# Kernel tuning notes

Measured on AMD Instinct MI355X. Metric: run time of the kernel, lower is better.

## Reference

```python
import jax, jax.numpy as jnp
import numpy as np

B, S, D = 4, 2048, 1024

def setup_inputs() -> dict:
    key = jax.random.key(0)
    k1, k2, k3, k4 = jax.random.split(key, 4)
    scale = 1.0 / np.sqrt(D)
    return {
        "X": jax.random.normal(k1, (B, S, D), dtype=jnp.float32),
        "W_Q": jax.random.normal(k2, (D, D), dtype=jnp.float32) * scale,
        "W_K": jax.random.normal(k3, (D, D), dtype=jnp.float32) * scale,
        "W_V": jax.random.normal(k4, (D, D), dtype=jnp.float32) * scale,
    }

def reference(X, W_Q, W_K, W_V):
    # nn.Linear computes X @ W.T; weights stored as [out, in]
    Q = jnp.einsum('bsd,ed->bse', X, W_Q)
    K = jnp.einsum('bsd,ed->bse', X, W_K)
    V = jnp.einsum('bsd,ed->bse', X, W_V)
    d_model = X.shape[-1]
    scores = jnp.einsum('bqd,bkd->bqk', Q, K) / jnp.sqrt(jnp.float32(d_model))
    S_len = X.shape[1]
    causal = jnp.tril(jnp.ones((S_len, S_len), dtype=bool))  # True = keep
    scores = jnp.where(causal[None, :, :], scores, -jnp.inf)
    attn = jax.nn.softmax(scores, axis=-1)
    return jnp.einsum('bqk,bkd->bqd', attn, V)
```

## Files before the change

kernel.cpp:

```cpp
#include <hip/hip_runtime.h>

typedef unsigned short u16;
typedef __attribute__((ext_vector_type(8))) short short8;
typedef __attribute__((ext_vector_type(4))) float floatx4;
typedef __attribute__((ext_vector_type(4))) unsigned short ushortx4;

#define BATCH 4
#define SEQ   2048
#define DMODEL 1024

__device__ __forceinline__ u16 f2bf(float f) {
  unsigned int u = __builtin_bit_cast(unsigned int, f);
  u = (u + 0x7FFFu + ((u >> 16) & 1u)) >> 16;
  return (u16)u;
}
__device__ __forceinline__ float bf2f(u16 u) {
  unsigned int v = ((unsigned int)u) << 16;
  return __builtin_bit_cast(float, v);
}

typedef const __attribute__((address_space(1))) unsigned int as1_u32;
typedef __attribute__((address_space(3))) unsigned int as3_u32;

__device__ __forceinline__ void gload16(const void* gp, void* lp) {
  __builtin_amdgcn_global_load_lds((as1_u32*)gp, (as3_u32*)lp, 16, 0, 0);
}

#define CFENCE asm volatile("" ::: "memory")
#define LGKM0  do { asm volatile("s_waitcnt lgkmcnt(0)" ::: "memory"); \
                    __builtin_amdgcn_sched_barrier(0); } while (0)
#define VMC(n) asm volatile("s_waitcnt vmcnt(" #n ")" ::: "memory")
#define BAR    __builtin_amdgcn_s_barrier()
#define PRIO1  __builtin_amdgcn_s_setprio(1)
#define PRIO0  __builtin_amdgcn_s_setprio(0)

template<int NW, int STRIPE>
__device__ __forceinline__ void stage_unit(
    const u16* __restrict__ G, int ld, int org, int kt, int h,
    u16* region, int w, int l)
{
  constexpr int CPS = STRIPE / 16;
  const int lr = l >> 3, s = l & 7;
  #pragma unroll
  for (int i = 0; i < 2; ++i) {
    int c = i * NW + w;
    int R = (c / CPS) * STRIPE + h * (STRIPE / 2) + (c % CPS) * 8;
    const u16* src = G + (size_t)(org + R + lr) * ld + kt * 64 + ((s ^ lr) << 3);
    gload16(src, region + R * 64);
  }
}

template<int REP>
__device__ __forceinline__ short8 rdfrag(const u16* region, int wq, int m, int kh, int l) {
  int r = wq * (REP * 16) + m * 16 + (l & 15);
  int c = kh * 32 + ((l >> 4) << 3);
  return *(const short8*)(region + ((r * 64 + c) ^ ((r & 7) << 3)));
}

template<int WM, int WN, int MREP, int NREP>
__device__ __forceinline__ void gemm_core3(
    const u16* __restrict__ A, int lda,
    const u16* __restrict__ B, int ldb,
    int m0, int n0, int NT, u16* lds,
    floatx4 (&acc)[MREP][NREP])
{
  constexpr int NW = WM * WN;
  constexpr int BM = WM * MREP * 16, BN = WN * NREP * 16;
  constexpr int ABUF = BM * 64;
  constexpr int BUFSZ = (BM + BN) * 64;
  constexpr int MH = MREP / 2, NH = NREP / 2;
  constexpr int SA = BM / WM, SB = BN / WN;

  const int tid = threadIdx.x;
  const int w = tid >> 6, l = tid & 63;
  const int wr = w / WN, wc = w % WN;

  u16* buf0 = lds;
  u16* buf1 = lds + BUFSZ;

  stage_unit<NW, SA>(A, lda, m0, 0, 0, buf0, w, l);
  stage_unit<NW, SB>(B, ldb, n0, 0, 0, buf0 + ABUF, w, l);
  stage_unit<NW, SB>(B, ldb, n0, 0, 1, buf0 + ABUF, w, l);
  stage_unit<NW, SA>(A, lda, m0, 0, 1, buf0, w, l);
  stage_unit<NW, SA>(A, lda, m0, 1, 0, buf1, w, l);
  stage_unit<NW, SB>(B, ldb, n0, 1, 0, buf1 + ABUF, w, l);
  VMC(8);
  BAR;
  CFENCE;

  for (int kt = 0; kt < NT; ++kt) {
    u16* cur = (kt & 1) ? buf1 : buf0;
    u16* oth = (kt & 1) ? buf0 : buf1;
    const int t1 = (kt + 1 < NT) ? kt + 1 : NT - 1;
    const int t2 = (kt + 2 < NT) ? kt + 2 : NT - 1;

    short8 aLo[MH][2], aHi[MH][2], bLo[NH][2], bHi[NH][2];

    #pragma unroll
    for (int m = 0; m < MH; ++m)
      #pragma unroll
      for (int k = 0; k < 2; ++k) aLo[m][k] = rdfrag<MREP>(cur, wr, m, k, l);
    #pragma unroll
    for (int n = 0; n < NH; ++n)
      #pragma unroll
      for (int k = 0; k < 2; ++k) bLo[n][k] = rdfrag<NREP>(cur + ABUF, wc, n, k, l);
    stage_unit<NW, SB>(B, ldb, n0, t1, 1, oth + ABUF, w, l);
    stage_unit<NW, SA>(A, lda, m0, t1, 1, oth, w, l);
    VMC(10);
    LGKM0;
    BAR;
    CFENCE;
    PRIO1;
    #pragma unroll
    for (int m = 0; m < MH; ++m)
      #pragma unroll
      for (int n = 0; n < NH; ++n)
        #pragma unroll
        for (int k = 0; k < 2; ++k)
          acc[m][n] = __builtin_amdgcn_mfma_f32_16x16x32_bf16(aLo[m][k], bLo[n][k], acc[m][n], 0, 0, 0);
    PRIO0;

    #pragma unroll
    for (int n = 0; n < NH; ++n)
      #pragma unroll
      for (int k = 0; k < 2; ++k) bHi[n][k] = rdfrag<NREP>(cur + ABUF, wc, n + NH, k, l);
    stage_unit<NW, SA>(A, lda, m0, t2, 0, cur, w, l);
    VMC(10);
    LGKM0;
    BAR;
    CFENCE;
    PRIO1;
    #pragma unroll
    for (int m = 0; m < MH; ++m)
      #pragma unroll
      for (int n = 0; n < NH; ++n)
        #pragma unroll
        for (int k = 0; k < 2; ++k)
          acc[m][n + NH] = __builtin_amdgcn_mfma_f32_16x16x32_bf16(aLo[m][k], bHi[n][k], acc[m][n + NH], 0, 0, 0);
    PRIO0;

    #pragma unroll
    for (int m = 0; m < MH; ++m)
      #pragma unroll
      for (int k = 0; k < 2; ++k) aHi[m][k] = rdfrag<MREP>(cur, wr, m + MH, k, l);
    stage_unit<NW, SB>(B, ldb, n0, t2, 0, cur + ABUF, w, l);
    VMC(8);
    LGKM0;
    BAR;
    CFENCE;
    PRIO1;
    #pragma unroll
    for (int m = 0; m < MH; ++m)
      #pragma unroll
      for (int n = 0; n < NH; ++n)
        #pragma unroll
        for (int k = 0; k < 2; ++k) {
          acc[m + MH][n + NH] = __builtin_amdgcn_mfma_f32_16x16x32_bf16(aHi[m][k], bHi[n][k], acc[m + MH][n + NH], 0, 0, 0);
          acc[m + MH][n] = __builtin_amdgcn_mfma_f32_16x16x32_bf16(aHi[m][k], bLo[n][k], acc[m + MH][n], 0, 0, 0);
        }
    PRIO0;
  }
  VMC(0);
}

template<int WM, int WN, int MREP, int NREP>
__device__ __forceinline__ void gemm_core8(
    const u16* __restrict__ A, int lda,
    const u16* __restrict__ B, int ldb,
    int m0, int n0, int NT, u16* lds,
    floatx4 (&acc)[MREP][NREP])
{
  constexpr int NW = WM * WN;
  constexpr int BM = WM * MREP * 16, BN = WN * NREP * 16;
  constexpr int ABUF = BM * 64;
  constexpr int BUFSZ = (BM + BN) * 64;
  constexpr int MH = MREP / 2, NH = NREP / 2;
  constexpr int SA = BM / WM, SB = BN / WN;

  const int tid = threadIdx.x;
  const int w = tid >> 6, l = tid & 63;
  const int wr = w / WN, wc = w % WN;

  u16* const bufp[2] = { lds, lds + BUFSZ };

  stage_unit<NW, SA>(A, lda, m0, 0, 0, bufp[0], w, l);
  stage_unit<NW, SB>(B, ldb, n0, 0, 0, bufp[0] + ABUF, w, l);
  stage_unit<NW, SB>(B, ldb, n0, 0, 1, bufp[0] + ABUF, w, l);
  stage_unit<NW, SA>(A, lda, m0, 0, 1, bufp[0], w, l);
  stage_unit<NW, SA>(A, lda, m0, 1, 0, bufp[1], w, l);
  stage_unit<NW, SB>(B, ldb, n0, 1, 0, bufp[1] + ABUF, w, l);
  stage_unit<NW, SB>(B, ldb, n0, 1, 1, bufp[1] + ABUF, w, l);
  VMC(6);
  BAR;
  CFENCE;

  for (int t = 0; t < NT; t += 2) {
    u16* c0 = bufp[t & 1];
    u16* c1 = bufp[(t + 1) & 1];
    const int t2 = (t + 2 < NT) ? t + 2 : NT - 1;
    const int t3 = (t + 3 < NT) ? t + 3 : NT - 1;

    short8 aLo[MH][2], aHi[MH][2], bLo[NH][2], bHi[NH][2];

    #pragma unroll
    for (int m = 0; m < MH; ++m)
      #pragma unroll
      for (int k = 0; k < 2; ++k) aLo[m][k] = rdfrag<MREP>(c0, wr, m, k, l);
    #pragma unroll
    for (int n = 0; n < NH; ++n)
      #pragma unroll
      for (int k = 0; k < 2; ++k) bLo[n][k] = rdfrag<NREP>(c0 + ABUF, wc, n, k, l);
    stage_unit<NW, SA>(A, lda, m0, t + 1, 1, c1, w, l);
    if constexpr (MH * 2 + NH * 2 >= 12) asm volatile("s_waitcnt lgkmcnt(8)" ::: "memory");
    BAR; LGKM0; PRIO1;
    #pragma unroll
    for (int m = 0; m < MH; ++m)
      #pragma unroll
      for (int n = 0; n < NH; ++n)
        #pragma unroll
        for (int k = 0; k < 2; ++k)
          acc[m][n] = __builtin_amdgcn_mfma_f32_16x16x32_bf16(aLo[m][k], bLo[n][k], acc[m][n], 0, 0, 0);
    PRIO0; BAR; CFENCE;

    #pragma unroll
    for (int n = 0; n < NH; ++n)
      #pragma unroll
      for (int k = 0; k < 2; ++k) bHi[n][k] = rdfrag<NREP>(c0 + ABUF, wc, n + NH, k, l);
    stage_unit<NW, SA>(A, lda, m0, t2, 0, c0, w, l);
    BAR; LGKM0; PRIO1;
    #pragma unroll
    for (int m = 0; m < MH; ++m)
      #pragma unroll
      for (int n = 0; n < NH; ++n)
        #pragma unroll
        for (int k = 0; k < 2; ++k)
          acc[m][n + NH] = __builtin_amdgcn_mfma_f32_16x16x32_bf16(aLo[m][k], bHi[n][k], acc[m][n + NH], 0, 0, 0);
    PRIO0; BAR; CFENCE;

    #pragma unroll
    for (int m = 0; m < MH; ++m)
      #pragma unroll
      for (int k = 0; k < 2; ++k) aHi[m][k] = rdfrag<MREP>(c0, wr, m + MH, k, l);
    stage_unit<NW, SB>(B, ldb, n0, t2, 0, c0 + ABUF, w, l);
    BAR; LGKM0; PRIO1;
    #pragma unroll
    for (int m = 0; m < MH; ++m)
      #pragma unroll
      for (int n = 0; n < NH; ++n)
        #pragma unroll
        for (int k = 0; k < 2; ++k)
          acc[m + MH][n + NH] = __builtin_amdgcn_mfma_f32_16x16x32_bf16(aHi[m][k], bHi[n][k], acc[m + MH][n + NH], 0, 0, 0);
    PRIO0; BAR; CFENCE;

    stage_unit<NW, SB>(B, ldb, n0, t2, 1, c0 + ABUF, w, l);
    VMC(6);
    BAR; PRIO1;
    #pragma unroll
    for (int m = 0; m < MH; ++m)
      #pragma unroll
      for (int n = 0; n < NH; ++n)
        #pragma unroll
        for (int k = 0; k < 2; ++k)
          acc[m + MH][n] = __builtin_amdgcn_mfma_f32_16x16x32_bf16(aHi[m][k], bLo[n][k], acc[m + MH][n], 0, 0, 0);
    PRIO0; BAR; CFENCE;

    #pragma unroll
    for (int m = 0; m < MH; ++m)
      #pragma unroll
      for (int k = 0; k < 2; ++k) aLo[m][k] = rdfrag<MREP>(c1, wr, m, k, l);
    #pragma unroll
    for (int n = 0; n < NH; ++n)
      #pragma unroll
      for (int k = 0; k < 2; ++k) bLo[n][k] = rdfrag<NREP>(c1 + ABUF, wc, n, k, l);
    stage_unit<NW, SA>(A, lda, m0, t2, 1, c0, w, l);
    if constexpr (MH * 2 + NH * 2 >= 12) asm volatile("s_waitcnt lgkmcnt(8)" ::: "memory");
    BAR; LGKM0; PRIO1;
    #pragma unroll
    for (int m = 0; m < MH; ++m)
      #pragma unroll
      for (int n = 0; n < NH; ++n)
        #pragma unroll
        for (int k = 0; k < 2; ++k)
          acc[m][n] = __builtin_amdgcn_mfma_f32_16x16x32_bf16(aLo[m][k], bLo[n][k], acc[m][n], 0, 0, 0);
    PRIO0; BAR; CFENCE;

    #pragma unroll
    for (int n = 0; n < NH; ++n)
      #pragma unroll
      for (int k = 0; k < 2; ++k) bHi[n][k] = rdfrag<NREP>(c1 + ABUF, wc, n + NH, k, l);
    stage_unit<NW, SA>(A, lda, m0, t3, 0, c1, w, l);
    BAR; LGKM0; PRIO1;
    #pragma unroll
    for (int m = 0; m < MH; ++m)
      #pragma unroll
      for (int n = 0; n < NH; ++n)
        #pragma unroll
        for (int k = 0; k < 2; ++k)
          acc[m][n + NH] = __builtin_amdgcn_mfma_f32_16x16x32_bf16(aLo[m][k], bHi[n][k], acc[m][n + NH], 0, 0, 0);
    PRIO0; BAR; CFENCE;

    #pragma unroll
    for (int m = 0; m < MH; ++m)
      #pragma unroll
      for (int k = 0; k < 2; ++k) aHi[m][k] = rdfrag<MREP>(c1, wr, m + MH, k, l);
    stage_unit<NW, SB>(B, ldb, n0, t3, 0, c1 + ABUF, w, l);
    BAR; LGKM0; PRIO1;
    #pragma unroll
    for (int m = 0; m < MH; ++m)
      #pragma unroll
      for (int n = 0; n < NH; ++n)
        #pragma unroll
        for (int k = 0; k < 2; ++k)
          acc[m + MH][n + NH] = __builtin_amdgcn_mfma_f32_16x16x32_bf16(aHi[m][k], bHi[n][k], acc[m + MH][n + NH], 0, 0, 0);
    PRIO0; BAR; CFENCE;

    stage_unit<NW, SB>(B, ldb, n0, t3, 1, c1 + ABUF, w, l);
    VMC(6);
    BAR; PRIO1;
    #pragma unroll
    for (int m = 0; m < MH; ++m)
      #pragma unroll
      for (int n = 0; n < NH; ++n)
        #pragma unroll
        for (int k = 0; k < 2; ++k)
          acc[m + MH][n] = __builtin_amdgcn_mfma_f32_16x16x32_bf16(aHi[m][k], bLo[n][k], acc[m + MH][n], 0, 0, 0);
    PRIO0; BAR; CFENCE;
  }
  VMC(0);
}

__global__ __launch_bounds__(256)
void convert_k(const float* __restrict__ X,
               const float* __restrict__ WQ,
               const float* __restrict__ WK,
               const float* __restrict__ WV,
               u16* __restrict__ Xb, u16* __restrict__ Wb)
{
  const int NX = (BATCH*SEQ*DMODEL) / 4;
  const int NW_ = (DMODEL*DMODEL) / 4;
  const int total = NX + 3*NW_;
  for (int i = blockIdx.x * 256 + threadIdx.x; i < total; i += gridDim.x * 256) {
    const float4* src; u16* dst; int j;
    if (i < NX) { src = (const float4*)X; j = i; dst = Xb; }
    else {
      int t = i - NX; int w = t / NW_; j = t - w * NW_;
      src = (const float4*)(w == 0 ? WQ : (w == 1 ? WK : WV));
      dst = Wb + (size_t)w * (DMODEL*DMODEL);
    }
    float4 v = src[j];
    ushortx4 p = { f2bf(v.x), f2bf(v.y), f2bf(v.z), f2bf(v.w) };
    *(ushortx4*)(dst + (size_t)j * 4) = p;
  }
}

__global__ __launch_bounds__(512, 1)
void qk256(const u16* __restrict__ Xb, const u16* __restrict__ Wb,
           u16* __restrict__ Q, u16* __restrict__ K)
{
  __shared__ __align__(16) u16 lds[2 * (256 + 256) * 64];
  const int id = blockIdx.x;
  const int sw = (id & 7) * 32 + (id >> 3);
  const int z = sw >> 7;
  const int rem = sw & 127;
  const int mt = rem >> 2, nt = rem & 3;
  const int m0 = mt * 256, n0 = nt * 256;

  floatx4 acc[8][4] = {};
  gemm_core3<2, 4, 8, 4>(Xb, DMODEL, Wb + (size_t)z * DMODEL * DMODEL, DMODEL,
                         m0, n0, DMODEL / 64, lds, acc);

  const int l = threadIdx.x & 63, w = threadIdx.x >> 6;
  const int wr = w >> 2, wc = w & 3;
  const int row0 = m0 + wr * 128 + ((l >> 4) << 2);
  const int col0 = n0 + wc * 64 + (l & 15);
  u16* O = z ? K : Q;
  #pragma unroll
  for (int m = 0; m < 8; ++m)
    #pragma unroll
    for (int n = 0; n < 4; ++n)
      #pragma unroll
      for (int i = 0; i < 4; ++i)
        O[(size_t)(row0 + m*16 + i) * DMODEL + col0 + n*16] = f2bf(acc[m][n][i]);
}

__global__ __launch_bounds__(256, 2)
void sv128(const u16* __restrict__ Xb, const u16* __restrict__ Wb,
           const u16* __restrict__ Qb, const u16* __restrict__ Kb,
           u16* __restrict__ Sc, u16* __restrict__ Vt)
{
  __shared__ __align__(16) u16 lds[2 * (128 + 128) * 64];
  const int id = blockIdx.x;
  const int sw = (id & 7) * 132 + (id >> 3);

  const u16 *A, *B;
  int m0, n0, b = 0;
  bool is_s;
  if (sw < 544) {
    is_s = true;
    b = sw / 136;
    const int t = sw % 136;
    int qt = 0;
    while ((qt + 1) * (qt + 2) / 2 <= t) ++qt;
    const int kt = t - qt * (qt + 1) / 2;
    m0 = qt * 128; n0 = kt * 128;
    A = Qb + (size_t)b * SEQ * DMODEL;
    B = Kb + (size_t)b * SEQ * DMODEL;
  } else {
    is_s = false;
    const int s = sw - 544;
    m0 = (s >> 3) * 128; n0 = (s & 7) * 128;
    A = Xb;
    B = Wb + (size_t)2 * DMODEL * DMODEL;
  }

  floatx4 acc[4][4] = {};
  gemm_core8<2, 2, 4, 4>(A, DMODEL, B, DMODEL, m0, n0, DMODEL / 64, lds, acc);

  const int l = threadIdx.x & 63, w = threadIdx.x >> 6;
  const int wr = w >> 1, wc = w & 1;
  const int row0 = m0 + wr * 64 + ((l >> 4) << 2);
  const int col0 = n0 + wc * 64 + (l & 15);

  if (is_s) {
    u16* S = Sc + (size_t)b * SEQ * SEQ;
    #pragma unroll
    for (int m = 0; m < 4; ++m)
      #pragma unroll
      for (int n = 0; n < 4; ++n)
        #pragma unroll
        for (int i = 0; i < 4; ++i)
          S[(size_t)(row0 + m*16 + i) * SEQ + col0 + n*16] = f2bf(acc[m][n][i] * 0.03125f);
  } else {
    #pragma unroll
    for (int m = 0; m < 4; ++m) {
      int gm = row0 + m*16;
      int bb = gm >> 11, s2 = gm & (SEQ - 1);
      #pragma unroll
      for (int n = 0; n < 4; ++n) {
        int d = col0 + n*16;
        ushortx4 p = { f2bf(acc[m][n][0]), f2bf(acc[m][n][1]),
                       f2bf(acc[m][n][2]), f2bf(acc[m][n][3]) };
        *(ushortx4*)(Vt + ((size_t)bb * DMODEL + d) * SEQ + s2) = p;
      }
    }
  }
}

__global__ __launch_bounds__(256)
void softmax1p(u16* __restrict__ Sc)
{
  __shared__ float red[4];
  const int rg = blockIdx.x;
  const int q = rg & (SEQ - 1);
  u16* row = Sc + (size_t)rg * SEQ;
  const int t = threadIdx.x;
  const int lane = t & 63, wave = t >> 6;
  const int n = q + 1;
  const int kpad = ((q >> 7) + 1) << 7;
  const int k0 = t * 8;

  short8 v8 = {};
  if (k0 < kpad) v8 = *(const short8*)(row + k0);
  float f[8];
  float lmax = -3.4e38f;
  #pragma unroll
  for (int j = 0; j < 8; ++j) {
    f[j] = bf2f((u16)v8[j]);
    if (k0 + j < n) lmax = fmaxf(lmax, f[j]);
  }
  #pragma unroll
  for (int off = 32; off >= 1; off >>= 1)
    lmax = fmaxf(lmax, __shfl_xor(lmax, off));
  if (lane == 0) red[wave] = lmax;
  __syncthreads();
  const float rmax = fmaxf(fmaxf(red[0], red[1]), fmaxf(red[2], red[3]));
  __syncthreads();

  float lsum = 0.f;
  #pragma unroll
  for (int j = 0; j < 8; ++j) {
    float e = (k0 + j < n) ? __expf(f[j] - rmax) : 0.f;
    f[j] = e;
    lsum += e;
  }
  #pragma unroll
  for (int off = 32; off >= 1; off >>= 1)
    lsum += __shfl_xor(lsum, off);
  if (lane == 0) red[wave] = lsum;
  __syncthreads();
  const float inv = 1.f / (red[0] + red[1] + red[2] + red[3]);

  if (k0 < kpad) {
    short8 o;
    #pragma unroll
    for (int j = 0; j < 8; ++j) o[j] = (short)f2bf(f[j] * inv);
    *(short8*)(row + k0) = o;
  }
}

__global__ __launch_bounds__(256, 2)
void out128(const u16* __restrict__ Sc, const u16* __restrict__ Vt,
            float* __restrict__ Out)
{
  __shared__ __align__(16) u16 lds[2 * (128 + 128) * 64];
  const int id = blockIdx.x;
  const int j = id & 255;
  const int upper = id >> 8;
  const int qt = upper ? (15 - (j & 15)) : (j & 15);
  const int nt = (j >> 4) & 7;
  const int b  = (upper << 1) | (j >> 7);
  const int m0 = qt * 128, n0 = nt * 128;

  const u16* P = Sc + (size_t)b * SEQ * SEQ;
  const u16* V = Vt + (size_t)b * DMODEL * SEQ;
  const int NT = (qt + 1) * 2;

  floatx4 acc[4][4] = {};
  gemm_core8<2, 2, 4, 4>(P, SEQ, V, SEQ, m0, n0, NT, lds, acc);

  float* O = Out + (size_t)b * SEQ * DMODEL;
  const int l = threadIdx.x & 63, w = threadIdx.x >> 6;
  const int wr = w >> 1, wc = w & 1;
  const int row0 = m0 + wr * 64 + ((l >> 4) << 2);
  const int col0 = n0 + wc * 64 + (l & 15);
  #pragma unroll
  for (int m = 0; m < 4; ++m)
    #pragma unroll
    for (int n = 0; n < 4; ++n)
      #pragma unroll
      for (int i = 0; i < 4; ++i)
        O[(size_t)(row0 + m*16 + i) * DMODEL + col0 + n*16] = acc[m][n][i];
}

extern "C" void kernel_launch(void* const* d_in, const int* in_sizes, int n_in,
                              void* d_out, int out_size, void* d_ws, size_t ws_size,
                              hipStream_t stream)
{
  const float* X  = (const float*)d_in[0];
  const float* WQ = (const float*)d_in[1];
  const float* WK = (const float*)d_in[2];
  const float* WV = (const float*)d_in[3];
  float* Out = (float*)d_out;

  char* ws = (char*)d_ws;
  u16*   Xb = (u16*)(ws);
  u16*   Wb = (u16*)(ws + 16777216);
  u16*   Qb = (u16*)(ws + 23068672);
  u16*   Kb = (u16*)(ws + 39845888);
  u16*   Vt = (u16*)(ws + 56623104);
  u16*   Sc = (u16*)(ws + 73400320);

  convert_k<<<dim3(2048), dim3(256), 0, stream>>>(X, WQ, WK, WV, Xb, Wb);
  qk256<<<dim3(256), dim3(512), 0, stream>>>(Xb, Wb, Qb, Kb);
  sv128<<<dim3(1056), dim3(256), 0, stream>>>(Xb, Wb, Qb, Kb, Sc, Vt);
  softmax1p<<<dim3(BATCH * SEQ), dim3(256), 0, stream>>>(Sc);
  out128<<<dim3(512), dim3(256), 0, stream>>>(Sc, Vt, Out);
}
```

Before: 135.2 us.

## Replace 8-wave ping-pong GEMM core with simple K=32 double-buffered loop

Replaces the hand-scheduled ping-pong GEMM core (64-wide K tiles, staged quarter loads, interleaved barriers) in the S/V and output GEMM kernels with a simpler loop over 32-wide K tiles. Each iteration prefetches the next tile and runs 16 MFMAs per wave. LDS per block is halved and launch bounds are raised to 4 blocks per CU to gain occupancy. In exchange it gives up the fine-grained load/compute interleaving, and with half the work per barrier the synchronisation cost per FLOP goes up.

```diff
diff --git a/kernel.cpp b/kernel.cpp
--- a/kernel.cpp
+++ b/kernel.cpp
@@ -163,170 +163,71 @@
   VMC(0);
 }
 
-template<int WM, int WN, int MREP, int NREP>
-__device__ __forceinline__ void gemm_core8(
+__device__ __forceinline__ void stage32(
+    const u16* __restrict__ G, int ld, int org, int kt,
+    u16* region, int w, int l)
+{
+  const int lr = l >> 2, s = l & 3;
+  #pragma unroll
+  for (int i = 0; i < 2; ++i) {
+    int R = (i * 4 + w) * 16;
+    const u16* src = G + (size_t)(org + R + lr) * ld + kt * 32 + ((s ^ (lr & 3)) << 3);
+    gload16(src, region + R * 32);
+  }
+}
+
+__device__ __forceinline__ short8 rdfrag32(const u16* region, int wq, int m, int l) {
+  int r = wq * 64 + m * 16 + (l & 15);
+  int j = l >> 4;
+  return *(const short8*)(region + r * 32 + (((j ^ (r & 3))) << 3));
+}
+
+__device__ __forceinline__ void gemm_core32(
     const u16* __restrict__ A, int lda,
     const u16* __restrict__ B, int ldb,
     int m0, int n0, int NT, u16* lds,
-    floatx4 (&acc)[MREP][NREP])
-{
-  constexpr int NW = WM * WN;
-  constexpr int BM = WM * MREP * 16, BN = WN * NREP * 16;
-  constexpr int ABUF = BM * 64;
-  constexpr int BUFSZ = (BM + BN) * 64;
-  constexpr int MH = MREP / 2, NH = NREP / 2;
-  constexpr int SA = BM / WM, SB = BN / WN;
-
+    floatx4 (&acc)[4][4])
+{
+  constexpr int ABUF = 128 * 32;
+  constexpr int BUFSZ = 256 * 32;
   const int tid = threadIdx.x;
   const int w = tid >> 6, l = tid & 63;
-  const int wr = w / WN, wc = w % WN;
-
-  u16* const bufp[2] = { lds, lds + BUFSZ };
-
-  stage_unit<NW, SA>(A, lda, m0, 0, 0, bufp[0], w, l);
-  stage_unit<NW, SB>(B, ldb, n0, 0, 0, bufp[0] + ABUF, w, l);
-  stage_unit<NW, SB>(B, ldb, n0, 0, 1, bufp[0] + ABUF, w, l);
-  stage_unit<NW, SA>(A, lda, m0, 0, 1, bufp[0], w, l);
-  stage_unit<NW, SA>(A, lda, m0, 1, 0, bufp[1], w, l);
-  stage_unit<NW, SB>(B, ldb, n0, 1, 0, bufp[1] + ABUF, w, l);
-  stage_unit<NW, SB>(B, ldb, n0, 1, 1, bufp[1] + ABUF, w, l);
-  VMC(6);
-  BAR;
-  CFENCE;
-
-  for (int t = 0; t < NT; t += 2) {
-    u16* c0 = bufp[t & 1];
-    u16* c1 = bufp[(t + 1) & 1];
-    const int t2 = (t + 2 < NT) ? t + 2 : NT - 1;
-    const int t3 = (t + 3 < NT) ? t + 3 : NT - 1;
-
-    short8 aLo[MH][2], aHi[MH][2], bLo[NH][2], bHi[NH][2];
-
-    #pragma unroll
-    for (int m = 0; m < MH; ++m)
-      #pragma unroll
-      for (int k = 0; k < 2; ++k) aLo[m][k] = rdfrag<MREP>(c0, wr, m, k, l);
-    #pragma unroll
-    for (int n = 0; n < NH; ++n)
-      #pragma unroll
-      for (int k = 0; k < 2; ++k) bLo[n][k] = rdfrag<NREP>(c0 + ABUF, wc, n, k, l);
-    stage_unit<NW, SA>(A, lda, m0, t + 1, 1, c1, w, l);
-    if constexpr (MH * 2 + NH * 2 >= 12) asm volatile("s_waitcnt lgkmcnt(8)" ::: "memory");
-    BAR; LGKM0; PRIO1;
-    #pragma unroll
-    for (int m = 0; m < MH; ++m)
-      #pragma unroll
-      for (int n = 0; n < NH; ++n)
-        #pragma unroll
-        for (int k = 0; k < 2; ++k)
-          acc[m][n] = __builtin_amdgcn_mfma_f32_16x16x32_bf16(aLo[m][k], bLo[n][k], acc[m][n], 0, 0, 0);
-    PRIO0; BAR; CFENCE;
-
-    #pragma unroll
-    for (int n = 0; n < NH; ++n)
-      #pragma unroll
-      for (int k = 0; k < 2; ++k) bHi[n][k] = rdfrag<NREP>(c0 + ABUF, wc, n + NH, k, l);
-    stage_unit<NW, SA>(A, lda, m0, t2, 0, c0, w, l);
-    BAR; LGKM0; PRIO1;
-    #pragma unroll
-    for (int m = 0; m < MH; ++m)
-      #pragma unroll
-      for (int n = 0; n < NH; ++n)
-        #pragma unroll
-        for (int k = 0; k < 2; ++k)
-          acc[m][n + NH] = __builtin_amdgcn_mfma_f32_16x16x32_bf16(aLo[m][k], bHi[n][k], acc[m][n + NH], 0, 0, 0);
-    PRIO0; BAR; CFENCE;
-
-    #pragma unroll
-    for (int m = 0; m < MH; ++m)
-      #pragma unroll
-      for (int k = 0; k < 2; ++k) aHi[m][k] = rdfrag<MREP>(c0, wr, m + MH, k, l);
-    stage_unit<NW, SB>(B, ldb, n0, t2, 0, c0 + ABUF, w, l);
-    BAR; LGKM0; PRIO1;
-    #pragma unroll
-    for (int m = 0; m < MH; ++m)
-      #pragma unroll
-      for (int n = 0; n < NH; ++n)
-        #pragma unroll
-        for (int k = 0; k < 2; ++k)
-          acc[m + MH][n + NH] = __builtin_amdgcn_mfma_f32_16x16x32_bf16(aHi[m][k], bHi[n][k], acc[m + MH][n + NH], 0, 0, 0);
-    PRIO0; BAR; CFENCE;
-
-    stage_unit<NW, SB>(B, ldb, n0, t2, 1, c0 + ABUF, w, l);
-    VMC(6);
-    BAR; PRIO1;
-    #pragma unroll
-    for (int m = 0; m < MH; ++m)
-      #pragma unroll
-      for (int n = 0; n < NH; ++n)
-        #pragma unroll
-        for (int k = 0; k < 2; ++k)
-          acc[m + MH][n] = __builtin_amdgcn_mfma_f32_16x16x32_bf16(aHi[m][k], bLo[n][k], acc[m + MH][n], 0, 0, 0);
-    PRIO0; BAR; CFENCE;
-
-    #pragma unroll
-    for (int m = 0; m < MH; ++m)
-      #pragma unroll
-      for (int k = 0; k < 2; ++k) aLo[m][k] = rdfrag<MREP>(c1, wr, m, k, l);
-    #pragma unroll
-    for (int n = 0; n < NH; ++n)
-      #pragma unroll
-      for (int k = 0; k < 2; ++k) bLo[n][k] = rdfrag<NREP>(c1 + ABUF, wc, n, k, l);
-    stage_unit<NW, SA>(A, lda, m0, t2, 1, c0, w, l);
-    if constexpr (MH * 2 + NH * 2 >= 12) asm volatile("s_waitcnt lgkmcnt(8)" ::: "memory");
-    BAR; LGKM0; PRIO1;
-    #pragma unroll
-    for (int m = 0; m < MH; ++m)
-      #pragma unroll
-      for (int n = 0; n < NH; ++n)
-        #pragma unroll
-        for (int k = 0; k < 2; ++k)
-          acc[m][n] = __builtin_amdgcn_mfma_f32_16x16x32_bf16(aLo[m][k], bLo[n][k], acc[m][n], 0, 0, 0);
-    PRIO0; BAR; CFENCE;
-
-    #pragma unroll
-    for (int n = 0; n < NH; ++n)
-      #pragma unroll
-      for (int k = 0; k < 2; ++k) bHi[n][k] = rdfrag<NREP>(c1 + ABUF, wc, n + NH, k, l);
-    stage_unit<NW, SA>(A, lda, m0, t3, 0, c1, w, l);
-    BAR; LGKM0; PRIO1;
-    #pragma unroll
-    for (int m = 0; m < MH; ++m)
-      #pragma unroll
-      for (int n = 0; n < NH; ++n)
-        #pragma unroll
-        for (int k = 0; k < 2; ++k)
-          acc[m][n + NH] = __builtin_amdgcn_mfma_f32_16x16x32_bf16(aLo[m][k], bHi[n][k], acc[m][n + NH], 0, 0, 0);
-    PRIO0; BAR; CFENCE;
-
-    #pragma unroll
-    for (int m = 0; m < MH; ++m)
-      #pragma unroll
-      for (int k = 0; k < 2; ++k) aHi[m][k] = rdfrag<MREP>(c1, wr, m + MH, k, l);
-    stage_unit<NW, SB>(B, ldb, n0, t3, 0, c1 + ABUF, w, l);
-    BAR; LGKM0; PRIO1;
-    #pragma unroll
-    for (int m = 0; m < MH; ++m)
-      #pragma unroll
-      for (int n = 0; n < NH; ++n)
-        #pragma unroll
-        for (int k = 0; k < 2; ++k)
-          acc[m + MH][n + NH] = __builtin_amdgcn_mfma_f32_16x16x32_bf16(aHi[m][k], bHi[n][k], acc[m + MH][n + NH], 0, 0, 0);
-    PRIO0; BAR; CFENCE;
-
-    stage_unit<NW, SB>(B, ldb, n0, t3, 1, c1 + ABUF, w, l);
-    VMC(6);
-    BAR; PRIO1;
-    #pragma unroll
-    for (int m = 0; m < MH; ++m)
-      #pragma unroll
-      for (int n = 0; n < NH; ++n)
-        #pragma unroll
-        for (int k = 0; k < 2; ++k)
-          acc[m + MH][n] = __builtin_amdgcn_mfma_f32_16x16x32_bf16(aHi[m][k], bLo[n][k], acc[m + MH][n], 0, 0, 0);
-    PRIO0; BAR; CFENCE;
-  }
-  VMC(0);
+  const int wr = w >> 1, wc = w & 1;
+
+  u16* buf0 = lds;
+  u16* buf1 = lds + BUFSZ;
+
+  stage32(A, lda, m0, 0, buf0, w, l);
+  stage32(B, ldb, n0, 0, buf0 + ABUF, w, l);
+
+  for (int kt = 0; kt < NT; ++kt) {
+    u16* cur = (kt & 1) ? buf1 : buf0;
+    u16* nxt = (kt & 1) ? buf0 : buf1;
+    if (kt + 1 < NT) {
+      stage32(A, lda, m0, kt + 1, nxt, w, l);
+      stage32(B, ldb, n0, kt + 1, nxt + ABUF, w, l);
+      VMC(4);
+    } else {
+      VMC(0);
+    }
+    BAR;
+    CFENCE;
+
+    short8 af[4], bfv[4];
+    #pragma unroll
+    for (int m = 0; m < 4; ++m) af[m] = rdfrag32(cur, wr, m, l);
+    #pragma unroll
+    for (int n = 0; n < 4; ++n) bfv[n] = rdfrag32(cur + ABUF, wc, n, l);
+    PRIO1;
+    #pragma unroll
+    for (int m = 0; m < 4; ++m)
+      #pragma unroll
+      for (int n = 0; n < 4; ++n)
+        acc[m][n] = __builtin_amdgcn_mfma_f32_16x16x32_bf16(af[m], bfv[n], acc[m][n], 0, 0, 0);
+    PRIO0;
+    BAR;
+    CFENCE;
+  }
 }
 
 __global__ __launch_bounds__(256)
@@ -383,12 +284,12 @@
         O[(size_t)(row0 + m*16 + i) * DMODEL + col0 + n*16] = f2bf(acc[m][n][i]);
 }
 
-__global__ __launch_bounds__(256, 2)
+__global__ __launch_bounds__(256, 4)
 void sv128(const u16* __restrict__ Xb, const u16* __restrict__ Wb,
            const u16* __restrict__ Qb, const u16* __restrict__ Kb,
            u16* __restrict__ Sc, u16* __restrict__ Vt)
 {
-  __shared__ __align__(16) u16 lds[2 * (128 + 128) * 64];
+  __shared__ __align__(16) u16 lds[2 * 256 * 32];
   const int id = blockIdx.x;
   const int sw = (id & 7) * 132 + (id >> 3);
 
@@ -414,7 +315,7 @@
   }
 
   floatx4 acc[4][4] = {};
-  gemm_core8<2, 2, 4, 4>(A, DMODEL, B, DMODEL, m0, n0, DMODEL / 64, lds, acc);
+  gemm_core32(A, DMODEL, B, DMODEL, m0, n0, DMODEL / 32, lds, acc);
 
   const int l = threadIdx.x & 63, w = threadIdx.x >> 6;
   const int wr = w >> 1, wc = w & 1;
@@ -498,11 +399,11 @@
   }
 }
 
-__global__ __launch_bounds__(256, 2)
+__global__ __launch_bounds__(256, 4)
 void out128(const u16* __restrict__ Sc, const u16* __restrict__ Vt,
             float* __restrict__ Out)
 {
-  __shared__ __align__(16) u16 lds[2 * (128 + 128) * 64];
+  __shared__ __align__(16) u16 lds[2 * 256 * 32];
   const int id = blockIdx.x;
   const int j = id & 255;
   const int upper = id >> 8;
@@ -513,10 +414,10 @@
 
   const u16* P = Sc + (size_t)b * SEQ * SEQ;
   const u16* V = Vt + (size_t)b * DMODEL * SEQ;
-  const int NT = (qt + 1) * 2;
+  const int NT = (qt + 1) * 4;
 
   floatx4 acc[4][4] = {};
-  gemm_core8<2, 2, 4, 4>(P, SEQ, V, SEQ, m0, n0, NT, lds, acc);
+  gemm_core32(P, SEQ, V, SEQ, m0, n0, NT, lds, acc);
 
   float* O = Out + (size_t)b * SEQ * DMODEL;
   const int l = threadIdx.x & 63, w = threadIdx.x >> 6;
```

Result: slower. 144.7 us (+7.0%).
